# Kernel optimization log

Hardware: AMD Instinct MI355X
Metric: run time of the kernel (lower is better)

Reference implementation:

```python
import jax, jax.numpy as jnp
import numpy as np

B, N = 16, 16          # batch, boxes per image
H, W = 640, 640        # image size
PH, PW = 300, 300      # learned patch size
MIN_AREA = 60.0
MAX_ANG = 20.0 * np.pi / 180.0


def setup_inputs() -> dict:
    key = jax.random.key(0)
    k1, k2, k3 = jax.random.split(key, 3)
    images = jax.random.uniform(k1, (B, H, W, 3), jnp.float32, -1.0, 1.0)
    patch = jax.random.uniform(k2, (PH, PW, 3), jnp.float32, -1.0, 1.0)
    kb1, kb2, kb3 = jax.random.split(k3, 3)
    ymin = jax.random.uniform(kb1, (B, N), jnp.float32, 0.0, H - 220.0)
    xmin = jax.random.uniform(kb2, (B, N), jnp.float32, 0.0, W - 220.0)
    hw = jax.random.uniform(kb3, (B, N, 2), jnp.float32, 100.0, 200.0)
    boxes = jnp.stack([ymin, xmin, ymin + hw[..., 0], xmin + hw[..., 1]], axis=-1)
    scale = jnp.float32(0.4)
    return {"boxes": boxes, "images": images, "patch": patch, "scale": scale}


def _bilinear(img, ys, xs):
    # img [Ph,Pw,3]; ys,xs [H,W] continuous source coords -> [H,W,3]
    Ph, Pw = img.shape[0], img.shape[1]
    y0 = jnp.floor(ys)
    x0 = jnp.floor(xs)
    wy = (ys - y0)[..., None]
    wx = (xs - x0)[..., None]
    y0i = jnp.clip(y0.astype(jnp.int32), 0, Ph - 1)
    y1i = jnp.clip(y0i + 1, 0, Ph - 1)
    x0i = jnp.clip(x0.astype(jnp.int32), 0, Pw - 1)
    x1i = jnp.clip(x0i + 1, 0, Pw - 1)
    v00 = img[y0i, x0i]
    v01 = img[y0i, x1i]
    v10 = img[y1i, x0i]
    v11 = img[y1i, x1i]
    return v00 * (1 - wy) * (1 - wx) + v01 * (1 - wy) * wx + v10 * wy * (1 - wx) + v11 * wy * wx


def _per_image(img, boxes_i, patch, scale, key):
    # random_print_adjust: per-channel affine jitter of the patch
    kw, kb, kloop = jax.random.split(key, 3)
    w = jax.random.normal(kw, (1, 1, 3), jnp.float32) * 0.1 + 0.5
    b = jax.random.normal(kb, (1, 1, 3), jnp.float32) * 0.01
    p = jnp.clip(w * patch + b, -1.0, 1.0)
    # BrightnessMatcher: shift patch mean brightness to match the image
    p = jnp.clip(p + (jnp.mean(img) - jnp.mean(p)), -1.0, 1.0)

    oimg = img
    mask0 = jnp.zeros_like(img)
    yy, xx = jnp.meshgrid(jnp.arange(H, dtype=jnp.float32),
                          jnp.arange(W, dtype=jnp.float32), indexing="ij")

    def step(carry, inp):
        image, mask = carry
        box, kk = inp
        ymin, xmin, ymax, xmax = box[0], box[1], box[2], box[3]
        h = ymax - ymin
        ww = xmax - xmin
        longer = jnp.maximum(h, ww)
        ps = jnp.floor(longer * scale)                       # patch_h == patch_w
        diag = jnp.minimum(jnp.sqrt(2.0).astype(jnp.float32) * ps, jnp.float32(W))
        oy = ymin + h / 2.0
        ox = xmin + ww / 2.0
        y0 = jnp.maximum(oy - diag / 2.0, 0.0)
        x0 = jnp.maximum(ox - diag / 2.0, 0.0)
        y0 = jnp.where(y0 + diag > H, H - diag, y0)
        x0 = jnp.where(x0 + diag > W, W - diag, x0)
        # int casts as in the TF code (values are >= 0, trunc == floor)
        y0i = jnp.floor(y0)
        x0i = jnp.floor(x0)
        phi = jnp.maximum(jnp.floor(ps), 1.0)
        diagi = jnp.floor(diag)
        valid_box = (phi * phi) > MIN_AREA

        k1, k2, k3 = jax.random.split(kk, 3)
        angle = jax.random.uniform(k1, (), jnp.float32, -MAX_ANG, MAX_ANG)

        # inverse warp: output pixel -> padded-patch coords -> resized-patch coords
        u = yy - y0i
        v = xx - x0i
        in_sq = (u >= 0) & (v >= 0) & (u < diagi) & (v < diagi)
        c = (diagi - 1.0) / 2.0
        ca, sa = jnp.cos(angle), jnp.sin(angle)
        su = c + ca * (u - c) - sa * (v - c)
        sv = c + sa * (u - c) + ca * (v - c)
        top = jnp.floor((diagi - phi) / 2.0)   # pad offset (floor top/left)
        py = su - top
        px = sv - top
        valid_src = (py >= 0) & (py <= phi - 1) & (px >= 0) & (px <= phi - 1)
        # resized-patch coords -> original patch coords (bilinear resize, half-pixel)
        sy = (py + 0.5) * (PH / phi) - 0.5
        sx = (px + 0.5) * (PW / phi) - 0.5
        samp = _bilinear(p, sy, sx)                                   # [H,W,3]
        noise = jax.random.uniform(k2, samp.shape, jnp.float32, -0.1, 0.1)
        bright = jax.random.uniform(k3, (), jnp.float32, -0.3, 0.3)
        im = jnp.clip(samp + noise + bright, -1.0, 1.0)
        val = jnp.where(valid_src[..., None], im, -2.0)
        val = jnp.where(val < -1.0, image, val)   # fill with current background
        val = jnp.clip(val, -1.0, 1.0)
        sel = (in_sq & valid_box)[..., None]
        new_image = jnp.where(sel, val, image)
        new_mask = jnp.where(sel, oimg - val, mask)
        return (new_image, new_mask), None

    keys = jax.random.split(kloop, N)
    (img_out, mask_out), _ = jax.lax.scan(step, (img, mask0), (boxes_i, keys))
    return img_out, mask_out


def reference(boxes, images, patch, scale):
    keys = jax.random.split(jax.random.key(42), B)
    img_out, mask_out = jax.vmap(_per_image, in_axes=(0, 0, None, None, 0))(
        images, boxes, patch, scale, keys)
    return img_out, mask_out
```

## Files before the change

kernel.cpp:

```cpp
#include <hip/hip_runtime.h>
#include <stdint.h>
#include <math.h>

#define B_ 16
#define N_ 16
#define H_ 640
#define W_ 640
#define PH_ 300
#define PW_ 300

#define IMG_ELEMS (H_*W_*3)
#define IMG_F4    (IMG_ELEMS/4)
#define PATCH_ELEMS (PH_*PW_*3)

typedef float fx4 __attribute__((ext_vector_type(4)));

__device__ __forceinline__ uint2 tf2x32(uint32_t k0, uint32_t k1, uint32_t x0, uint32_t x1) {
  uint32_t k2 = k0 ^ k1 ^ 0x1BD11BDAu;
#define TFR(r) x0 += x1; x1 = (x1 << (r)) | (x1 >> (32 - (r))); x1 ^= x0;
  x0 += k0; x1 += k1;
  TFR(13) TFR(15) TFR(26) TFR(6)
  x0 += k1; x1 += k2 + 1u;
  TFR(17) TFR(29) TFR(16) TFR(24)
  x0 += k2; x1 += k0 + 2u;
  TFR(13) TFR(15) TFR(26) TFR(6)
  x0 += k0; x1 += k1 + 3u;
  TFR(17) TFR(29) TFR(16) TFR(24)
  x0 += k1; x1 += k2 + 4u;
  TFR(13) TFR(15) TFR(26) TFR(6)
  x0 += k2; x1 += k0 + 5u;
#undef TFR
  return make_uint2(x0, x1);
}

__device__ __forceinline__ uint32_t rb32(uint32_t k0, uint32_t k1, uint32_t i) {
  uint2 o = tf2x32(k0, k1, 0u, i);
  return o.x ^ o.y;
}

__device__ __forceinline__ float u01f(uint32_t bits) {
  return __uint_as_float((bits >> 9) | 0x3F800000u) - 1.0f;
}

__device__ __forceinline__ float erfinv32(float x) {
  float w = -log1pf(-x * x);
  float p;
  if (w < 5.0f) {
    w = w - 2.5f;
    p = 2.81022636e-08f;
    p = fmaf(p, w, 3.43273939e-07f);
    p = fmaf(p, w, -3.5233877e-06f);
    p = fmaf(p, w, -4.39150654e-06f);
    p = fmaf(p, w, 0.00021858087f);
    p = fmaf(p, w, -0.00125372503f);
    p = fmaf(p, w, -0.00417768164f);
    p = fmaf(p, w, 0.246640727f);
    p = fmaf(p, w, 1.50140941f);
  } else {
    w = sqrtf(w) - 3.0f;
    p = -0.000200214257f;
    p = fmaf(p, w, 0.000100950558f);
    p = fmaf(p, w, 0.00134934322f);
    p = fmaf(p, w, -0.00367342844f);
    p = fmaf(p, w, 0.00573950773f);
    p = fmaf(p, w, -0.0076224613f);
    p = fmaf(p, w, 0.00943887047f);
    p = fmaf(p, w, 1.00167406f);
    p = fmaf(p, w, 2.83297682f);
  }
  return p * x;
}

__device__ __forceinline__ float jnormal(uint32_t bits) {
  float lo = __uint_as_float(0xBF7FFFFFu);
  float span = 1.0f - lo;
  float u = fmaxf(lo, u01f(bits) * span + lo);
  return 1.4142135623730951f * erfinv32(u);
}

__global__ void setup_kernel(const float* __restrict__ boxes, const float* __restrict__ scale_p,
                             float* __restrict__ params, float* __restrict__ wb) {
  int t = threadIdx.x;
  if (t >= B_*N_) return;
  int b = t >> 4, n = t & 15;
  uint2 kb = tf2x32(0u, 42u, 0u, (uint32_t)b);
  uint2 kw  = tf2x32(kb.x, kb.y, 0u, 0u);
  uint2 kbk = tf2x32(kb.x, kb.y, 0u, 1u);
  uint2 kl  = tf2x32(kb.x, kb.y, 0u, 2u);
  if (n == 0) {
    wb[b*8+0] = jnormal(rb32(kw.x,  kw.y,  0u)) * 0.1f + 0.5f;
    wb[b*8+1] = jnormal(rb32(kw.x,  kw.y,  1u)) * 0.1f + 0.5f;
    wb[b*8+2] = jnormal(rb32(kw.x,  kw.y,  2u)) * 0.1f + 0.5f;
    wb[b*8+3] = jnormal(rb32(kbk.x, kbk.y, 0u)) * 0.01f;
    wb[b*8+4] = jnormal(rb32(kbk.x, kbk.y, 1u)) * 0.01f;
    wb[b*8+5] = jnormal(rb32(kbk.x, kbk.y, 2u)) * 0.01f;
  }
  uint2 kk = tf2x32(kl.x, kl.y, 0u, (uint32_t)n);
  uint2 k1 = tf2x32(kk.x, kk.y, 0u, 0u);
  uint2 k2 = tf2x32(kk.x, kk.y, 0u, 1u);
  uint2 k3 = tf2x32(kk.x, kk.y, 0u, 2u);
  const float MA = (float)(20.0 * 3.14159265358979323846 / 180.0);
  float angle  = fmaxf(-MA,   u01f(rb32(k1.x, k1.y, 0u)) * (MA - (-MA)) + (-MA));
  float bright = fmaxf(-0.3f, u01f(rb32(k3.x, k3.y, 0u)) * (0.3f - (-0.3f)) + (-0.3f));

  const float* bx = boxes + (size_t)t * 4;
  float ymin = bx[0], xmin = bx[1], ymax = bx[2], xmax = bx[3];
  float sc = scale_p[0];
  float h = ymax - ymin, ww = xmax - xmin;
  float longer = fmaxf(h, ww);
  float ps = floorf(longer * sc);
  float diag = fminf(sqrtf(2.0f) * ps, (float)W_);
  float oy = ymin + h * 0.5f;
  float ox = xmin + ww * 0.5f;
  float y0 = fmaxf(oy - diag * 0.5f, 0.0f);
  float x0 = fmaxf(ox - diag * 0.5f, 0.0f);
  if (y0 + diag > (float)H_) y0 = (float)H_ - diag;
  if (x0 + diag > (float)W_) x0 = (float)W_ - diag;
  float y0i = floorf(y0), x0i = floorf(x0);
  float phi = fmaxf(floorf(ps), 1.0f);
  float diagi = floorf(diag);
  float validf = ((phi * phi) > 60.0f) ? 1.0f : 0.0f;
  float c = (diagi - 1.0f) * 0.5f;
  float top = floorf((diagi - phi) * 0.5f);

  float* P = params + t * 16;
  P[0] = y0i; P[1] = x0i; P[2] = diagi; P[3] = phi;
  P[4] = c;
  P[5] = (float)cos((double)angle);
  P[6] = (float)sin((double)angle);
  P[7] = top;
  P[8] = bright; P[9] = (float)PH_ / phi; P[10] = 0.0f; P[11] = validf;
  P[12] = __uint_as_float(k2.x); P[13] = __uint_as_float(k2.y); P[14] = 0.0f; P[15] = 0.0f;
}

__global__ __launch_bounds__(256) void reduce_kernel(
    const float* __restrict__ images, const float* __restrict__ patch,
    const float* __restrict__ wb, double* __restrict__ partials) {
  int b = blockIdx.y, j = blockIdx.x, t = threadIdx.x;
  const fx4* img4 = (const fx4*)(images + (size_t)b * IMG_ELEMS);
  double s = 0.0;
  for (int i = j * 256 + t; i < IMG_F4; i += 64 * 256) {
    fx4 v = img4[i];
    s += (double)v.x + (double)v.y + (double)v.z + (double)v.w;
  }
  float w0 = wb[b*8+0], w1 = wb[b*8+1], w2 = wb[b*8+2];
  float b0 = wb[b*8+3], b1 = wb[b*8+4], b2 = wb[b*8+5];
  double sp = 0.0;
  for (int i = j * 256 + t; i < PATCH_ELEMS; i += 64 * 256) {
    int q = i / 3; int ch = i - q * 3;
    float wv = (ch == 0) ? w0 : ((ch == 1) ? w1 : w2);
    float bv = (ch == 0) ? b0 : ((ch == 1) ? b1 : b2);
    float pv = fminf(fmaxf(wv * patch[i] + bv, -1.0f), 1.0f);
    sp += (double)pv;
  }
  __shared__ double sh[256];
  sh[t] = s; __syncthreads();
  for (int o = 128; o > 0; o >>= 1) { if (t < o) sh[t] += sh[t + o]; __syncthreads(); }
  if (t == 0) partials[((size_t)b * 64 + j) * 2 + 0] = sh[0];
  __syncthreads();
  sh[t] = sp; __syncthreads();
  for (int o = 128; o > 0; o >>= 1) { if (t < o) sh[t] += sh[t + o]; __syncthreads(); }
  if (t == 0) partials[((size_t)b * 64 + j) * 2 + 1] = sh[0];
}

__global__ __launch_bounds__(256) void main_kernel(
    const float* __restrict__ images, const float* __restrict__ patch,
    const float* __restrict__ params, const float* __restrict__ wb,
    const double* __restrict__ partials, float* __restrict__ out) {
  __shared__ float sP[N_ * 16];
  __shared__ float sWB[6];
  __shared__ double sRed[64];
  __shared__ float sD;
  int b = blockIdx.y;
  int tid = threadIdx.x;
  if (tid < N_ * 16) sP[tid] = params[b * N_ * 16 + tid];
  if (tid < 6) sWB[tid] = wb[b * 8 + tid];
  if (tid < 64) {
    sRed[tid] = partials[((size_t)b * 64 + tid) * 2 + 0];
  }
  __syncthreads();
  if (tid < 32) { sRed[tid] += sRed[tid + 32]; }
  __syncthreads();
  if (tid == 0) {
    double si = 0.0;
    for (int j = 0; j < 32; j++) si += sRed[j];
    double sp = 0.0;
    for (int j = 0; j < 64; j++) sp += partials[((size_t)b * 64 + j) * 2 + 1];
    sD = (float)(si / (double)IMG_ELEMS) - (float)(sp / (double)PATCH_ELEMS);
  }
  __syncthreads();

  int g = blockIdx.x * 256 + tid;
  int p0 = g * 4;
  int y = p0 / W_;
  int x0p = p0 - y * W_;
  size_t base = ((size_t)b * (H_ * W_) + (size_t)p0) * 3;
  const fx4* in4 = (const fx4*)(images + base);
  fx4 L0 = in4[0], L1 = in4[1], L2 = in4[2];
  float pix[12];
  pix[0]=L0.x; pix[1]=L0.y; pix[2]=L0.z; pix[3]=L0.w;
  pix[4]=L1.x; pix[5]=L1.y; pix[6]=L1.z; pix[7]=L1.w;
  pix[8]=L2.x; pix[9]=L2.y; pix[10]=L2.z; pix[11]=L2.w;
  float img[12], mk[12];
#pragma unroll
  for (int i = 0; i < 12; i++) { img[i] = pix[i]; mk[i] = 0.0f; }
  float dsh = sD;
  float yf = (float)y;

#pragma unroll
  for (int j = 0; j < 4; j++) {
    float xf = (float)(x0p + j);
    float* oj = pix + j * 3;
    float* ij = img + j * 3;
    float* mj = mk + j * 3;
    for (int n = 0; n < N_; n++) {
      const float* P = sP + n * 16;
      if (P[11] == 0.0f) continue;
      float u = yf - P[0];
      float v = xf - P[1];
      float diagi = P[2];
      if (!(u >= 0.0f && v >= 0.0f && u < diagi && v < diagi)) continue;
      float phi = P[3], c = P[4], ca = P[5], sa = P[6], top = P[7], bright = P[8], sph = P[9];
      float t1 = u - c, t2 = v - c;
      float su = c + ca * t1 - sa * t2;
      float sv = c + sa * t1 + ca * t2;
      float py = su - top;
      float px = sv - top;
      bool vsrc = (py >= 0.0f) && (py <= phi - 1.0f) && (px >= 0.0f) && (px <= phi - 1.0f);
      if (vsrc) {
        float sy = (py + 0.5f) * sph - 0.5f;
        float sx = (px + 0.5f) * sph - 0.5f;
        float fy = floorf(sy), fx = floorf(sx);
        float wy = sy - fy, wxv = sx - fx;
        int iy0 = min(max((int)fy, 0), PH_ - 1);
        int iy1 = min(iy0 + 1, PH_ - 1);
        int ix0 = min(max((int)fx, 0), PW_ - 1);
        int ix1 = min(ix0 + 1, PW_ - 1);
        int o00 = (iy0 * PW_ + ix0) * 3;
        int o01 = (iy0 * PW_ + ix1) * 3;
        int o10 = (iy1 * PW_ + ix0) * 3;
        int o11 = (iy1 * PW_ + ix1) * 3;
        uint32_t k2a = __float_as_uint(P[12]);
        uint32_t k2b = __float_as_uint(P[13]);
        float omwy = 1.0f - wy, omwx = 1.0f - wxv;
        int nbase = (p0 + j) * 3;
#pragma unroll
        for (int ch = 0; ch < 3; ch++) {
          float wv = sWB[ch], bv = sWB[3 + ch];
          float a00 = fminf(fmaxf(wv * patch[o00 + ch] + bv, -1.0f), 1.0f);
          float a01 = fminf(fmaxf(wv * patch[o01 + ch] + bv, -1.0f), 1.0f);
          float a10 = fminf(fmaxf(wv * patch[o10 + ch] + bv, -1.0f), 1.0f);
          float a11 = fminf(fmaxf(wv * patch[o11 + ch] + bv, -1.0f), 1.0f);
          a00 = fminf(fmaxf(a00 + dsh, -1.0f), 1.0f);
          a01 = fminf(fmaxf(a01 + dsh, -1.0f), 1.0f);
          a10 = fminf(fmaxf(a10 + dsh, -1.0f), 1.0f);
          a11 = fminf(fmaxf(a11 + dsh, -1.0f), 1.0f);
          float samp = ((a00 * omwy) * omwx) + ((a01 * omwy) * wxv)
                     + ((a10 * wy) * omwx) + ((a11 * wy) * wxv);
          uint32_t bits = rb32(k2a, k2b, (uint32_t)(nbase + ch));
          float nz = fmaxf(-0.1f, u01f(bits) * (0.1f - (-0.1f)) + (-0.1f));
          float imv = fminf(fmaxf((samp + nz) + bright, -1.0f), 1.0f);
          ij[ch] = imv;
          mj[ch] = oj[ch] - imv;
        }
      } else {
#pragma unroll
        for (int ch = 0; ch < 3; ch++) mj[ch] = oj[ch] - ij[ch];
      }
    }
  }
  size_t moff = (size_t)B_ * (H_ * W_) * 3;
  fx4* oi4 = (fx4*)(out + base);
  fx4* om4 = (fx4*)(out + moff + base);
  fx4 S0 = {img[0], img[1], img[2],  img[3]};
  fx4 S1 = {img[4], img[5], img[6],  img[7]};
  fx4 S2 = {img[8], img[9], img[10], img[11]};
  fx4 M0 = {mk[0], mk[1], mk[2],  mk[3]};
  fx4 M1 = {mk[4], mk[5], mk[6],  mk[7]};
  fx4 M2 = {mk[8], mk[9], mk[10], mk[11]};
  __builtin_nontemporal_store(S0, oi4 + 0);
  __builtin_nontemporal_store(S1, oi4 + 1);
  __builtin_nontemporal_store(S2, oi4 + 2);
  __builtin_nontemporal_store(M0, om4 + 0);
  __builtin_nontemporal_store(M1, om4 + 1);
  __builtin_nontemporal_store(M2, om4 + 2);
}

extern "C" void kernel_launch(void* const* d_in, const int* in_sizes, int n_in,
                              void* d_out, int out_size, void* d_ws, size_t ws_size,
                              hipStream_t stream) {
  const float* boxes  = (const float*)d_in[0];
  const float* images = (const float*)d_in[1];
  const float* patch  = (const float*)d_in[2];
  const float* scale  = (const float*)d_in[3];
  float* out = (float*)d_out;

  float* params = (float*)d_ws;
  float* wb     = params + B_ * N_ * 16;
  double* partials = (double*)((char*)d_ws + 20480);

  setup_kernel<<<1, 256, 0, stream>>>(boxes, scale, params, wb);
  reduce_kernel<<<dim3(64, B_), 256, 0, stream>>>(images, patch, wb, partials);
  main_kernel<<<dim3((H_ * W_) / (256 * 4), B_), 256, 0, stream>>>(images, patch, params, wb, partials, out);
}
```

Baseline: 328.7 us.

## Fuse background copy into reduction pass and compose only box-overlapping tiles

The reduction kernel now also writes the image copy and a zero mask, so the full-image output pass disappears. The compose kernel runs on 16x16 tiles, builds a bitmask of boxes that overlap each tile, and exits early for tiles with none. Inside a tile it walks the boxes from last to first and only computes the final valid box for each pixel, skipping sampling for boxes that would be overwritten. The trade-offs are scalar, non-vectorised stores in box regions, extra reads of the original image there, and a small per-tile setup cost.

```diff
diff --git a/kernel.cpp b/kernel.cpp
--- a/kernel.cpp
+++ b/kernel.cpp
@@ -133,15 +133,21 @@
   P[12] = __uint_as_float(k2.x); P[13] = __uint_as_float(k2.y); P[14] = 0.0f; P[15] = 0.0f;
 }
 
-__global__ __launch_bounds__(256) void reduce_kernel(
+__global__ __launch_bounds__(256) void copy_reduce_kernel(
     const float* __restrict__ images, const float* __restrict__ patch,
-    const float* __restrict__ wb, double* __restrict__ partials) {
+    const float* __restrict__ wb, double* __restrict__ partials,
+    float* __restrict__ out) {
   int b = blockIdx.y, j = blockIdx.x, t = threadIdx.x;
   const fx4* img4 = (const fx4*)(images + (size_t)b * IMG_ELEMS);
+  fx4* oi4 = (fx4*)(out + (size_t)b * IMG_ELEMS);
+  fx4* om4 = (fx4*)(out + (size_t)B_ * IMG_ELEMS + (size_t)b * IMG_ELEMS);
+  const fx4 zero = {0.0f, 0.0f, 0.0f, 0.0f};
   double s = 0.0;
   for (int i = j * 256 + t; i < IMG_F4; i += 64 * 256) {
     fx4 v = img4[i];
     s += (double)v.x + (double)v.y + (double)v.z + (double)v.w;
+    __builtin_nontemporal_store(v, oi4 + i);
+    __builtin_nontemporal_store(zero, om4 + i);
   }
   float w0 = wb[b*8+0], w1 = wb[b*8+1], w2 = wb[b*8+2];
   float b0 = wb[b*8+3], b1 = wb[b*8+4], b2 = wb[b*8+5];
@@ -163,7 +169,7 @@
   if (t == 0) partials[((size_t)b * 64 + j) * 2 + 1] = sh[0];
 }
 
-__global__ __launch_bounds__(256) void main_kernel(
+__global__ __launch_bounds__(256) void compose_kernel(
     const float* __restrict__ images, const float* __restrict__ patch,
     const float* __restrict__ params, const float* __restrict__ wb,
     const double* __restrict__ partials, float* __restrict__ out) {
@@ -171,15 +177,28 @@
   __shared__ float sWB[6];
   __shared__ double sRed[64];
   __shared__ float sD;
-  int b = blockIdx.y;
+  int b = blockIdx.z;
   int tid = threadIdx.x;
   if (tid < N_ * 16) sP[tid] = params[b * N_ * 16 + tid];
   if (tid < 6) sWB[tid] = wb[b * 8 + tid];
-  if (tid < 64) {
-    sRed[tid] = partials[((size_t)b * 64 + tid) * 2 + 0];
-  }
-  __syncthreads();
-  if (tid < 32) { sRed[tid] += sRed[tid + 32]; }
+  __syncthreads();
+
+  int tx0 = blockIdx.x * 16;
+  int ty0 = blockIdx.y * 16;
+  unsigned bmask = 0;
+#pragma unroll
+  for (int n = 0; n < N_; n++) {
+    const float* P = sP + n * 16;
+    if (P[11] == 0.0f) continue;
+    int by0 = (int)P[0], bx0 = (int)P[1], d = (int)P[2];
+    if (bx0 < tx0 + 16 && bx0 + d > tx0 && by0 < ty0 + 16 && by0 + d > ty0)
+      bmask |= (1u << n);
+  }
+  if (bmask == 0) return;
+
+  if (tid < 64) sRed[tid] = partials[((size_t)b * 64 + tid) * 2 + 0];
+  __syncthreads();
+  if (tid < 32) sRed[tid] += sRed[tid + 32];
   __syncthreads();
   if (tid == 0) {
     double si = 0.0;
@@ -189,101 +208,67 @@
     sD = (float)(si / (double)IMG_ELEMS) - (float)(sp / (double)PATCH_ELEMS);
   }
   __syncthreads();
-
-  int g = blockIdx.x * 256 + tid;
-  int p0 = g * 4;
-  int y = p0 / W_;
-  int x0p = p0 - y * W_;
-  size_t base = ((size_t)b * (H_ * W_) + (size_t)p0) * 3;
-  const fx4* in4 = (const fx4*)(images + base);
-  fx4 L0 = in4[0], L1 = in4[1], L2 = in4[2];
-  float pix[12];
-  pix[0]=L0.x; pix[1]=L0.y; pix[2]=L0.z; pix[3]=L0.w;
-  pix[4]=L1.x; pix[5]=L1.y; pix[6]=L1.z; pix[7]=L1.w;
-  pix[8]=L2.x; pix[9]=L2.y; pix[10]=L2.z; pix[11]=L2.w;
-  float img[12], mk[12];
+  float dsh = sD;
+
+  int x = tx0 + (tid & 15);
+  int y = ty0 + (tid >> 4);
+  float xf = (float)x, yf = (float)y;
+  int p = y * W_ + x;
+
+  for (int n = N_ - 1; n >= 0; n--) {
+    if (!(bmask & (1u << n))) continue;
+    const float* P = sP + n * 16;
+    float u = yf - P[0];
+    float v = xf - P[1];
+    float diagi = P[2];
+    if (!(u >= 0.0f && v >= 0.0f && u < diagi && v < diagi)) continue;
+    float phi = P[3], c = P[4], ca = P[5], sa = P[6], top = P[7], bright = P[8], sph = P[9];
+    float t1 = u - c, t2 = v - c;
+    float su = c + ca * t1 - sa * t2;
+    float sv = c + sa * t1 + ca * t2;
+    float py = su - top;
+    float px = sv - top;
+    if (!((py >= 0.0f) && (py <= phi - 1.0f) && (px >= 0.0f) && (px <= phi - 1.0f))) continue;
+
+    float sy = (py + 0.5f) * sph - 0.5f;
+    float sx = (px + 0.5f) * sph - 0.5f;
+    float fy = floorf(sy), fx = floorf(sx);
+    float wy = sy - fy, wxv = sx - fx;
+    int iy0 = min(max((int)fy, 0), PH_ - 1);
+    int iy1 = min(iy0 + 1, PH_ - 1);
+    int ix0 = min(max((int)fx, 0), PW_ - 1);
+    int ix1 = min(ix0 + 1, PW_ - 1);
+    int o00 = (iy0 * PW_ + ix0) * 3;
+    int o01 = (iy0 * PW_ + ix1) * 3;
+    int o10 = (iy1 * PW_ + ix0) * 3;
+    int o11 = (iy1 * PW_ + ix1) * 3;
+    uint32_t k2a = __float_as_uint(P[12]);
+    uint32_t k2b = __float_as_uint(P[13]);
+    float omwy = 1.0f - wy, omwx = 1.0f - wxv;
+    size_t base = ((size_t)b * (H_ * W_) + (size_t)p) * 3;
+    size_t moff = (size_t)B_ * IMG_ELEMS;
 #pragma unroll
-  for (int i = 0; i < 12; i++) { img[i] = pix[i]; mk[i] = 0.0f; }
-  float dsh = sD;
-  float yf = (float)y;
-
-#pragma unroll
-  for (int j = 0; j < 4; j++) {
-    float xf = (float)(x0p + j);
-    float* oj = pix + j * 3;
-    float* ij = img + j * 3;
-    float* mj = mk + j * 3;
-    for (int n = 0; n < N_; n++) {
-      const float* P = sP + n * 16;
-      if (P[11] == 0.0f) continue;
-      float u = yf - P[0];
-      float v = xf - P[1];
-      float diagi = P[2];
-      if (!(u >= 0.0f && v >= 0.0f && u < diagi && v < diagi)) continue;
-      float phi = P[3], c = P[4], ca = P[5], sa = P[6], top = P[7], bright = P[8], sph = P[9];
-      float t1 = u - c, t2 = v - c;
-      float su = c + ca * t1 - sa * t2;
-      float sv = c + sa * t1 + ca * t2;
-      float py = su - top;
-      float px = sv - top;
-      bool vsrc = (py >= 0.0f) && (py <= phi - 1.0f) && (px >= 0.0f) && (px <= phi - 1.0f);
-      if (vsrc) {
-        float sy = (py + 0.5f) * sph - 0.5f;
-        float sx = (px + 0.5f) * sph - 0.5f;
-        float fy = floorf(sy), fx = floorf(sx);
-        float wy = sy - fy, wxv = sx - fx;
-        int iy0 = min(max((int)fy, 0), PH_ - 1);
-        int iy1 = min(iy0 + 1, PH_ - 1);
-        int ix0 = min(max((int)fx, 0), PW_ - 1);
-        int ix1 = min(ix0 + 1, PW_ - 1);
-        int o00 = (iy0 * PW_ + ix0) * 3;
-        int o01 = (iy0 * PW_ + ix1) * 3;
-        int o10 = (iy1 * PW_ + ix0) * 3;
-        int o11 = (iy1 * PW_ + ix1) * 3;
-        uint32_t k2a = __float_as_uint(P[12]);
-        uint32_t k2b = __float_as_uint(P[13]);
-        float omwy = 1.0f - wy, omwx = 1.0f - wxv;
-        int nbase = (p0 + j) * 3;
-#pragma unroll
-        for (int ch = 0; ch < 3; ch++) {
-          float wv = sWB[ch], bv = sWB[3 + ch];
-          float a00 = fminf(fmaxf(wv * patch[o00 + ch] + bv, -1.0f), 1.0f);
-          float a01 = fminf(fmaxf(wv * patch[o01 + ch] + bv, -1.0f), 1.0f);
-          float a10 = fminf(fmaxf(wv * patch[o10 + ch] + bv, -1.0f), 1.0f);
-          float a11 = fminf(fmaxf(wv * patch[o11 + ch] + bv, -1.0f), 1.0f);
-          a00 = fminf(fmaxf(a00 + dsh, -1.0f), 1.0f);
-          a01 = fminf(fmaxf(a01 + dsh, -1.0f), 1.0f);
-          a10 = fminf(fmaxf(a10 + dsh, -1.0f), 1.0f);
-          a11 = fminf(fmaxf(a11 + dsh, -1.0f), 1.0f);
-          float samp = ((a00 * omwy) * omwx) + ((a01 * omwy) * wxv)
-                     + ((a10 * wy) * omwx) + ((a11 * wy) * wxv);
-          uint32_t bits = rb32(k2a, k2b, (uint32_t)(nbase + ch));
-          float nz = fmaxf(-0.1f, u01f(bits) * (0.1f - (-0.1f)) + (-0.1f));
-          float imv = fminf(fmaxf((samp + nz) + bright, -1.0f), 1.0f);
-          ij[ch] = imv;
-          mj[ch] = oj[ch] - imv;
-        }
-      } else {
-#pragma unroll
-        for (int ch = 0; ch < 3; ch++) mj[ch] = oj[ch] - ij[ch];
-      }
+    for (int ch = 0; ch < 3; ch++) {
+      float wv = sWB[ch], bv = sWB[3 + ch];
+      float a00 = fminf(fmaxf(wv * patch[o00 + ch] + bv, -1.0f), 1.0f);
+      float a01 = fminf(fmaxf(wv * patch[o01 + ch] + bv, -1.0f), 1.0f);
+      float a10 = fminf(fmaxf(wv * patch[o10 + ch] + bv, -1.0f), 1.0f);
+      float a11 = fminf(fmaxf(wv * patch[o11 + ch] + bv, -1.0f), 1.0f);
+      a00 = fminf(fmaxf(a00 + dsh, -1.0f), 1.0f);
+      a01 = fminf(fmaxf(a01 + dsh, -1.0f), 1.0f);
+      a10 = fminf(fmaxf(a10 + dsh, -1.0f), 1.0f);
+      a11 = fminf(fmaxf(a11 + dsh, -1.0f), 1.0f);
+      float samp = ((a00 * omwy) * omwx) + ((a01 * omwy) * wxv)
+                 + ((a10 * wy) * omwx) + ((a11 * wy) * wxv);
+      uint32_t bits = rb32(k2a, k2b, (uint32_t)(p * 3 + ch));
+      float nz = fmaxf(-0.1f, u01f(bits) * (0.1f - (-0.1f)) + (-0.1f));
+      float imv = fminf(fmaxf((samp + nz) + bright, -1.0f), 1.0f);
+      float orig = images[base + ch];
+      out[base + ch] = imv;
+      out[moff + base + ch] = orig - imv;
     }
-  }
-  size_t moff = (size_t)B_ * (H_ * W_) * 3;
-  fx4* oi4 = (fx4*)(out + base);
-  fx4* om4 = (fx4*)(out + moff + base);
-  fx4 S0 = {img[0], img[1], img[2],  img[3]};
-  fx4 S1 = {img[4], img[5], img[6],  img[7]};
-  fx4 S2 = {img[8], img[9], img[10], img[11]};
-  fx4 M0 = {mk[0], mk[1], mk[2],  mk[3]};
-  fx4 M1 = {mk[4], mk[5], mk[6],  mk[7]};
-  fx4 M2 = {mk[8], mk[9], mk[10], mk[11]};
-  __builtin_nontemporal_store(S0, oi4 + 0);
-  __builtin_nontemporal_store(S1, oi4 + 1);
-  __builtin_nontemporal_store(S2, oi4 + 2);
-  __builtin_nontemporal_store(M0, om4 + 0);
-  __builtin_nontemporal_store(M1, om4 + 1);
-  __builtin_nontemporal_store(M2, om4 + 2);
+    return;
+  }
 }
 
 extern "C" void kernel_launch(void* const* d_in, const int* in_sizes, int n_in,
@@ -300,6 +285,6 @@
   double* partials = (double*)((char*)d_ws + 20480);
 
   setup_kernel<<<1, 256, 0, stream>>>(boxes, scale, params, wb);
-  reduce_kernel<<<dim3(64, B_), 256, 0, stream>>>(images, patch, wb, partials);
-  main_kernel<<<dim3((H_ * W_) / (256 * 4), B_), 256, 0, stream>>>(images, patch, params, wb, partials, out);
-}
+  copy_reduce_kernel<<<dim3(64, B_), 256, 0, stream>>>(images, patch, wb, partials, out);
+  compose_kernel<<<dim3(W_ / 16, H_ / 16, B_), 256, 0, stream>>>(images, patch, params, wb, partials, out);
+}
```

New measurement: 327.1 us. No clear change (-0.5%).
